# Performance work log

Measured on AMD Instinct MI355X. Metric: run time of the kernel, lower is better.

## Reference

```python
import jax, jax.numpy as jnp
import numpy as np

B, N, D_MODEL, LAP = 64, 64, 256, 16


def setup_inputs() -> dict:
    key = jax.random.key(0)
    ks = jax.random.split(key, 8)
    adj = jax.random.randint(ks[0], (B, N, N), 0, 2, dtype=jnp.int32)
    node_feats = jax.random.normal(ks[1], (B, N, D_MODEL), dtype=jnp.float32)
    eigvec = jax.random.normal(ks[2], (B, N, LAP), dtype=jnp.float32)
    W_lap = jax.random.normal(ks[3], (LAP, D_MODEL), dtype=jnp.float32) / np.sqrt(LAP)
    W_edge = jax.random.normal(ks[4], (1 + 2 * LAP, D_MODEL), dtype=jnp.float32) / np.sqrt(1 + 2 * LAP)
    b_edge = jax.random.normal(ks[5], (D_MODEL,), dtype=jnp.float32) * 0.02
    type_embed = jax.random.normal(ks[6], (2, D_MODEL), dtype=jnp.float32)
    graph_tok = jax.random.normal(ks[7], (1, 1, D_MODEL), dtype=jnp.float32)
    return {"adj": adj, "node_feats": node_feats, "eigvec": eigvec,
            "W_lap": W_lap, "W_edge": W_edge, "b_edge": b_edge,
            "type_embed": type_embed, "graph_tok": graph_tok}


def reference(adj, node_feats, eigvec, W_lap, W_edge, b_edge, type_embed, graph_tok):
    b, n, _ = adj.shape
    d = graph_tok.shape[-1]
    # node tokens: feats + LapPE projection
    node_tok = node_feats + jnp.einsum('bnl,ld->bnd', eigvec, W_lap)
    # upper-triangular candidate edges (fixed M = n(n-1)/2, jit-friendly)
    iu, ju = jnp.triu_indices(n, k=1)               # [M]
    valid = adj[:, iu, ju] > 0                       # [B, M]
    # stable compaction: valid edges first (matches torch per-graph extraction order)
    order = jnp.argsort(~valid, axis=1, stable=True) # [B, M]
    src = iu[order]                                  # [B, M]
    dst = ju[order]
    valid_sorted = jnp.take_along_axis(valid, order, axis=1)
    Pu = jnp.take_along_axis(eigvec, src[..., None], axis=1)  # [B, M, LAP]
    Pv = jnp.take_along_axis(eigvec, dst[..., None], axis=1)
    m = src.shape[1]
    edge_in = jnp.concatenate([jnp.ones((b, m, 1), eigvec.dtype), Pu, Pv], axis=-1)
    etok = jnp.einsum('bmf,fd->bmd', edge_in, W_edge) + b_edge + type_embed[1]
    etok = jnp.where(valid_sorted[..., None], etok, 0.0)      # zeros at padding
    pad_mask_edges = ~valid_sorted                             # True = padding
    gtok = jnp.broadcast_to(graph_tok, (b, 1, d))
    seq_embeds = jnp.concatenate([gtok, node_tok, etok], axis=1)  # [B, 1+n+M, d]
    pad_mask = jnp.concatenate([jnp.zeros((b, 1 + n), bool), pad_mask_edges], axis=1)
    return seq_embeds, pad_mask
```

## Files before the change

### kernel.cpp

```cpp
#include <hip/hip_runtime.h>

#define B_ 64
#define N_ 64
#define D_ 256
#define LAP_ 16
#define M_ 2016
#define TOK_ 2081

typedef float v4f __attribute__((ext_vector_type(4)));

__device__ __forceinline__ void ij_from_m(int m, int& i, int& j) {
    float fm = (float)m;
    int gi = (int)((127.0f - sqrtf(127.0f * 127.0f - 8.0f * fm)) * 0.5f);
    if (gi < 0) gi = 0;
    if (gi > 62) gi = 62;
    while (gi > 0 && (127 * gi - gi * gi) / 2 > m) gi--;
    while (gi < 62 && (127 * (gi + 1) - (gi + 1) * (gi + 1)) / 2 <= m) gi++;
    i = gi;
    j = gi + 1 + (m - (127 * gi - gi * gi) / 2);
}

__global__ __launch_bounds__(256, 2) void fused_kernel(
    const int*   __restrict__ adj,
    const float* __restrict__ node_feats,
    const float* __restrict__ eigvec,
    const float* __restrict__ W_lap,
    const float* __restrict__ W_edge,
    const float* __restrict__ b_edge,
    const float* __restrict__ type_embed,
    const float* __restrict__ graph_tok,
    float*       __restrict__ out)
{
    __shared__ float sEig[N_ * LAP_];
    __shared__ unsigned long long sWords[32];
    __shared__ int sTok[32];

    const int b = blockIdx.x;
    const int y = blockIdx.y;
    const int t = threadIdx.x;
    const int wave = t >> 6, lane = t & 63;
    const int c = t;

    ((float4*)sEig)[t] = ((const float4*)(eigvec + (size_t)b * N_ * LAP_))[t];

    if (y == 63) {
        float wl[LAP_];
#pragma unroll
        for (int l = 0; l < LAP_; l++) wl[l] = W_lap[l * D_ + c];
        __syncthreads();
        float* outB = out + (size_t)b * TOK_ * D_;
#pragma unroll 4
        for (int n = 0; n < N_; n++) {
            float a = node_feats[((size_t)b * N_ + n) * D_ + c];
            const float* e = sEig + n * LAP_;
#pragma unroll
            for (int l = 0; l < LAP_; l++) a += e[l] * wl[l];
            __builtin_nontemporal_store(a, outB + (size_t)(1 + n) * D_ + c);
        }
        outB[t] = graph_tok[t];
        if (t < 1 + N_)
            out[(size_t)B_ * TOK_ * D_ + (size_t)b * TOK_ + t] = 0.0f;
        return;
    }

#pragma unroll
    for (int k = 0; k < 8; k++) {
        int m = k * 256 + t;
        int valid = 0;
        if (m < M_) {
            int i, j;
            ij_from_m(m, i, j);
            valid = (adj[b * (N_ * N_) + i * N_ + j] > 0) ? 1 : 0;
        }
        unsigned long long blt = __ballot(valid);
        if (lane == 0) sWords[k * 4 + wave] = blt;
    }

    float base = W_edge[c] + b_edge[c] + type_embed[D_ + c];
    float w1[LAP_], w2[LAP_];
#pragma unroll
    for (int l = 0; l < LAP_; l++) {
        w1[l] = W_edge[(1 + l) * D_ + c];
        w2[l] = W_edge[(1 + LAP_ + l) * D_ + c];
    }
    __syncthreads();

    if (t < 32) {
        unsigned long long word = sWords[t];
        int cnt = __popcll(word);
        int inc = cnt;
#pragma unroll
        for (int off = 1; off < 32; off <<= 1) {
            int v = __shfl_up(inc, off);
            if (lane >= off) inc += v;
        }
        int pref  = inc - cnt;
        int total = __shfl(inc, 31);
        int m = y * 32 + t;
        int w = m >> 6, r = m & 63;
        unsigned long long ww = __shfl(word, w);
        int pw = __shfl(pref, w);
        int rank = pw + __popcll(ww & ((1ull << r) - 1ull));
        int valid = (int)((ww >> r) & 1ull);
        int p = valid ? rank : total + (m - rank);
        int i, j;
        ij_from_m(m, i, j);
        sTok[t] = i | (j << 6) | (valid << 12) | (p << 13);
        out[(size_t)B_ * TOK_ * D_ + (size_t)b * TOK_ + 1 + N_ + p] =
            valid ? 0.0f : 1.0f;
    }
    __syncthreads();

    float* outE = out + (size_t)b * TOK_ * D_ + (size_t)(1 + N_) * D_;
#pragma unroll 2
    for (int k = 0; k < 32; k++) {
        int info = sTok[k];
        int p = info >> 13;
        float acc = 0.0f;
        if (info & (1 << 12)) {
            int si = info & 63, di = (info >> 6) & 63;
            const v4f* eu4 = (const v4f*)(sEig + si * LAP_);
            const v4f* ev4 = (const v4f*)(sEig + di * LAP_);
            acc = base;
#pragma unroll
            for (int q = 0; q < 4; q++) {
                v4f u = eu4[q];
                v4f v = ev4[q];
                acc += u.x * w1[q * 4 + 0] + v.x * w2[q * 4 + 0];
                acc += u.y * w1[q * 4 + 1] + v.y * w2[q * 4 + 1];
                acc += u.z * w1[q * 4 + 2] + v.z * w2[q * 4 + 2];
                acc += u.w * w1[q * 4 + 3] + v.w * w2[q * 4 + 3];
            }
        }
        __builtin_nontemporal_store(acc, outE + (size_t)p * D_ + c);
    }
}

extern "C" void kernel_launch(void* const* d_in, const int* in_sizes, int n_in,
                              void* d_out, int out_size, void* d_ws, size_t ws_size,
                              hipStream_t stream) {
    const int*   adj        = (const int*)d_in[0];
    const float* node_feats = (const float*)d_in[1];
    const float* eigvec     = (const float*)d_in[2];
    const float* W_lap      = (const float*)d_in[3];
    const float* W_edge     = (const float*)d_in[4];
    const float* b_edge     = (const float*)d_in[5];
    const float* type_embed = (const float*)d_in[6];
    const float* graph_tok  = (const float*)d_in[7];
    float* out = (float*)d_out;

    fused_kernel<<<dim3(B_, 64), dim3(256), 0, stream>>>(
        adj, node_feats, eigvec, W_lap, W_edge, b_edge, type_embed, graph_tok, out);
}
```

Before: 193.8 us.

## Precompute per-node edge projections and repartition grid by channel groups

The edge projection is split algebraically into per-node terms U = eigvec·W1 and V = eigvec·W2, computed once per graph into shared memory. Each edge then needs only base + U[src] + V[dst] instead of a 32-term dot product. The grid changes from 64 edge-chunk blocks per graph to 4 channel-group blocks per graph, with each block handling all edges for 64 channels. Node tokens are folded into every block, so the separate node-token block is gone. The grid is far smaller (256 blocks), and larger shared memory use may reduce occupancy, while each thread's stores now hit 64-channel (256-byte) segments per row.

```diff
diff --git a/kernel.cpp b/kernel.cpp
--- a/kernel.cpp
+++ b/kernel.cpp
@@ -6,8 +6,6 @@
 #define LAP_ 16
 #define M_ 2016
 #define TOK_ 2081
-
-typedef float v4f __attribute__((ext_vector_type(4)));
 
 __device__ __forceinline__ void ij_from_m(int m, int& i, int& j) {
     float fm = (float)m;
@@ -32,56 +30,49 @@
     float*       __restrict__ out)
 {
     __shared__ float sEig[N_ * LAP_];
+    __shared__ float sU[N_ * 64];
+    __shared__ float sV[N_ * 64];
+    __shared__ int   sDest[M_];
     __shared__ unsigned long long sWords[32];
-    __shared__ int sTok[32];
+    __shared__ int sPref[32];
+    __shared__ int sTotal;
 
-    const int b = blockIdx.x;
-    const int y = blockIdx.y;
-    const int t = threadIdx.x;
+    const int b    = blockIdx.x;
+    const int cg   = blockIdx.y;
+    const int t    = threadIdx.x;
     const int wave = t >> 6, lane = t & 63;
-    const int c = t;
+    const int c    = cg * 64 + lane;
 
     ((float4*)sEig)[t] = ((const float4*)(eigvec + (size_t)b * N_ * LAP_))[t];
 
-    if (y == 63) {
-        float wl[LAP_];
+    int ival[8];
+    int av[8];
 #pragma unroll
-        for (int l = 0; l < LAP_; l++) wl[l] = W_lap[l * D_ + c];
-        __syncthreads();
-        float* outB = out + (size_t)b * TOK_ * D_;
-#pragma unroll 4
-        for (int n = 0; n < N_; n++) {
-            float a = node_feats[((size_t)b * N_ + n) * D_ + c];
-            const float* e = sEig + n * LAP_;
+    for (int k = 0; k < 8; k++) {
+        int m = k * 256 + t;
+        int i = 0, j = 0;
+        if (m < M_) {
+            ij_from_m(m, i, j);
+            av[k] = adj[b * (N_ * N_) + i * N_ + j];
+        } else av[k] = 0;
+        ival[k] = i | (j << 6);
+    }
+
+    float base = W_edge[c] + b_edge[c] + type_embed[D_ + c];
+    float w1c[LAP_], w2c[LAP_], wlc[LAP_];
 #pragma unroll
-            for (int l = 0; l < LAP_; l++) a += e[l] * wl[l];
-            __builtin_nontemporal_store(a, outB + (size_t)(1 + n) * D_ + c);
-        }
-        outB[t] = graph_tok[t];
-        if (t < 1 + N_)
-            out[(size_t)B_ * TOK_ * D_ + (size_t)b * TOK_ + t] = 0.0f;
-        return;
+    for (int l = 0; l < LAP_; l++) {
+        w1c[l] = W_edge[(1 + l) * D_ + c];
+        w2c[l] = W_edge[(1 + LAP_ + l) * D_ + c];
+        wlc[l] = W_lap[l * D_ + c];
     }
 
 #pragma unroll
     for (int k = 0; k < 8; k++) {
-        int m = k * 256 + t;
-        int valid = 0;
-        if (m < M_) {
-            int i, j;
-            ij_from_m(m, i, j);
-            valid = (adj[b * (N_ * N_) + i * N_ + j] > 0) ? 1 : 0;
-        }
+        int valid = (k * 256 + t < M_) && (av[k] > 0);
         unsigned long long blt = __ballot(valid);
         if (lane == 0) sWords[k * 4 + wave] = blt;
-    }
-
-    float base = W_edge[c] + b_edge[c] + type_embed[D_ + c];
-    float w1[LAP_], w2[LAP_];
-#pragma unroll
-    for (int l = 0; l < LAP_; l++) {
-        w1[l] = W_edge[(1 + l) * D_ + c];
-        w2[l] = W_edge[(1 + LAP_ + l) * D_ + c];
+        ival[k] |= valid << 12;
     }
     __syncthreads();
 
@@ -94,45 +85,68 @@
             int v = __shfl_up(inc, off);
             if (lane >= off) inc += v;
         }
-        int pref  = inc - cnt;
-        int total = __shfl(inc, 31);
-        int m = y * 32 + t;
-        int w = m >> 6, r = m & 63;
-        unsigned long long ww = __shfl(word, w);
-        int pw = __shfl(pref, w);
-        int rank = pw + __popcll(ww & ((1ull << r) - 1ull));
-        int valid = (int)((ww >> r) & 1ull);
-        int p = valid ? rank : total + (m - rank);
-        int i, j;
-        ij_from_m(m, i, j);
-        sTok[t] = i | (j << 6) | (valid << 12) | (p << 13);
-        out[(size_t)B_ * TOK_ * D_ + (size_t)b * TOK_ + 1 + N_ + p] =
-            valid ? 0.0f : 1.0f;
+        sPref[t] = inc - cnt;
+        if (t == 31) sTotal = inc;
+    }
+
+#pragma unroll 2
+    for (int n16 = 0; n16 < 16; n16++) {
+        int n = wave * 16 + n16;
+        const float* e = sEig + n * LAP_;
+        float accU = 0.0f, accV = 0.0f;
+#pragma unroll
+        for (int l = 0; l < LAP_; l++) {
+            float el = e[l];
+            accU += el * w1c[l];
+            accV += el * w2c[l];
+        }
+        sU[n * 64 + lane] = accU;
+        sV[n * 64 + lane] = accV;
     }
     __syncthreads();
 
-    float* outE = out + (size_t)b * TOK_ * D_ + (size_t)(1 + N_) * D_;
+    const int total = sTotal;
+    float* maskb = out + (size_t)B_ * TOK_ * D_ + (size_t)b * TOK_;
+#pragma unroll
+    for (int k = 0; k < 8; k++) {
+        int m = k * 256 + t;
+        if (m < M_) {
+            int w = k * 4 + wave;
+            unsigned long long word = sWords[w];
+            int rank = sPref[w] + __popcll(word & ((1ull << lane) - 1ull));
+            int valid = (ival[k] >> 12) & 1;
+            int p = valid ? rank : total + (m - rank);
+            sDest[m] = (ival[k] & 0xFFF) | (valid << 12) | (p << 13);
+            if (cg == 0) maskb[1 + N_ + p] = valid ? 0.0f : 1.0f;
+        }
+    }
+
+    float* outB = out + (size_t)b * TOK_ * D_;
 #pragma unroll 2
-    for (int k = 0; k < 32; k++) {
-        int info = sTok[k];
+    for (int n16 = 0; n16 < 16; n16++) {
+        int n = wave * 16 + n16;
+        float a = node_feats[((size_t)b * N_ + n) * D_ + c];
+        const float* e = sEig + n * LAP_;
+#pragma unroll
+        for (int l = 0; l < LAP_; l++) a += e[l] * wlc[l];
+        __builtin_nontemporal_store(a, outB + (size_t)(1 + n) * D_ + c);
+    }
+    if (wave == 0) outB[c] = graph_tok[c];
+    if (cg == 0 && t < 1 + N_) maskb[t] = 0.0f;
+    __syncthreads();
+
+    float* outE = outB + (size_t)(1 + N_) * D_;
+#pragma unroll 4
+    for (int q = 0; q < M_ / 4; q++) {
+        int m = wave * (M_ / 4) + q;
+        int info = sDest[m];
         int p = info >> 13;
-        float acc = 0.0f;
+        float val = 0.0f;
         if (info & (1 << 12)) {
             int si = info & 63, di = (info >> 6) & 63;
-            const v4f* eu4 = (const v4f*)(sEig + si * LAP_);
-            const v4f* ev4 = (const v4f*)(sEig + di * LAP_);
-            acc = base;
-#pragma unroll
-            for (int q = 0; q < 4; q++) {
-                v4f u = eu4[q];
-                v4f v = ev4[q];
-                acc += u.x * w1[q * 4 + 0] + v.x * w2[q * 4 + 0];
-                acc += u.y * w1[q * 4 + 1] + v.y * w2[q * 4 + 1];
-                acc += u.z * w1[q * 4 + 2] + v.z * w2[q * 4 + 2];
-                acc += u.w * w1[q * 4 + 3] + v.w * w2[q * 4 + 3];
-            }
+            val = base + sU[si * 64 + lane] + sV[di * 64 + lane];
         }
-        __builtin_nontemporal_store(acc, outE + (size_t)p * D_ + c);
+        __builtin_nontemporal_store(val, outE + (size_t)p * D_ + c);
     }
 }
 
@@ -149,6 +163,6 @@
     const float* graph_tok  = (const float*)d_in[7];
     float* out = (float*)d_out;
 
-    fused_kernel<<<dim3(B_, 64), dim3(256), 0, stream>>>(
+    fused_kernel<<<dim3(B_, 4), dim3(256), 0, stream>>>(
         adj, node_feats, eigvec, W_lap, W_edge, b_edge, type_embed, graph_tok, out);
 }
```

Result: faster. 187.4 us (-3.3%).
